# Performance work log

Measured on AMD Instinct MI355X. Metric: run time of the kernel, lower is better.

Reference implementation:

```python
import jax, jax.numpy as jnp
import numpy as np


def _lstm_layer(x, w_ih, w_hh, b, h0, c0):
    # x: [S, B, H]; w_ih, w_hh: [4H, H]; b: [4H] (b_ih + b_hh combined)
    H = h0.shape[-1]

    def step(carry, xt):
        h, c = carry
        gates = xt @ w_ih.T + h @ w_hh.T + b  # [B, 4H]
        i = jax.nn.sigmoid(gates[:, 0 * H:1 * H])
        f = jax.nn.sigmoid(gates[:, 1 * H:2 * H])
        g = jnp.tanh(gates[:, 2 * H:3 * H])
        o = jax.nn.sigmoid(gates[:, 3 * H:4 * H])
        c = f * c + i * g
        h = o * jnp.tanh(c)
        return (h, c), h

    (_, _), hs = jax.lax.scan(step, (h0, c0), x)
    return hs  # [S, B, H]


def setup_inputs() -> dict:
    key = jax.random.key(0)
    ks = jax.random.split(key, 5)
    S, B, H, L, C = 256, 64, 1024, 2, 10
    return {
        "x_data": jax.random.normal(ks[0], (S, B, H), dtype=jnp.float32),
        "weight": jax.random.normal(ks[1], (L, 2, 4 * H, H), dtype=jnp.float32) * 0.05,
        "bias": jax.random.normal(ks[2], (L, 2, 4 * H), dtype=jnp.float32) * 0.05,
        "fc_w": jax.random.normal(ks[3], (C, H), dtype=jnp.float32) * 0.05,
        "fc_b": jax.random.normal(ks[4], (C,), dtype=jnp.float32) * 0.05,
        "hiddenSize": H,
        "miniBatch": B,
        "seqLength": S,
        "numLayers": L,
    }


def reference(x_data, weight, bias, fc_w, fc_b, hiddenSize, miniBatch, seqLength, numLayers):
    B, H = miniBatch, hiddenSize
    h0 = jnp.zeros((B, H), dtype=x_data.dtype)
    c0 = jnp.zeros((B, H), dtype=x_data.dtype)
    x = x_data
    for layer in range(numLayers):
        w_ih = weight[layer, 0]  # [4H, H]
        w_hh = weight[layer, 1]  # [4H, H]
        b = bias[layer, 0] + bias[layer, 1]  # [4H]
        x = _lstm_layer(x, w_ih, w_hh, b, h0, c0)
    out = x[-1]  # last timestep of top layer: [B, H]
    return out @ fc_w.T + fc_b  # [B, num_classes]
```

## Files before the change

kernel.cpp:

```cpp
#include <hip/hip_runtime.h>
#include <cstdint>
#include <cstddef>

#define S_LEN 256
#define BATCH 64
#define HID   1024
#define GATES 4096
#define NBLK  256
#define RING_D 4

typedef _Float16 h16;
typedef _Float16 h16x8 __attribute__((ext_vector_type(8)));
typedef _Float16 h16x4 __attribute__((ext_vector_type(4)));
typedef float    f32x4 __attribute__((ext_vector_type(4)));

__global__ __launch_bounds__(256)
void xconv_kernel(const float* __restrict__ x, h16* __restrict__ x16)
{
  const int n4 = S_LEN * BATCH * HID / 4;
  const int stride = gridDim.x * 256;
  for (int i = blockIdx.x * 256 + threadIdx.x; i < n4; i += stride) {
    f32x4 v = ((const f32x4*)x)[i];
    h16x4 o;
    o[0] = (h16)v[0]; o[1] = (h16)v[1]; o[2] = (h16)v[2]; o[3] = (h16)v[3];
    ((h16x4*)x16)[i] = o;
  }
}

#define RLOAD(dst, ptr, OFFSTR)                                         \
  asm volatile("global_load_dwordx4 %0, %1, off offset:" OFFSTR " sc1"  \
               : "=&v"(dst) : "v"(ptr) : "memory")

__device__ __forceinline__ void wave_poll_c(const unsigned* grp, unsigned tgt)
{
  const unsigned* p = grp + (threadIdx.x & 63);
  while (true) {
    const unsigned u = __hip_atomic_load(p, __ATOMIC_RELAXED,
                                         __HIP_MEMORY_SCOPE_AGENT);
    if ((u & 0xffffu) >= tgt && (u >> 16) >= tgt) break;
    __builtin_amdgcn_s_sleep(1);
  }
}

__global__ __launch_bounds__(512, 1)
void lstm_persistent(const h16* __restrict__ x16,
                     const float* __restrict__ weight,
                     const float* __restrict__ bias,
                     h16* __restrict__ h0r,
                     h16* __restrict__ h1r,
                     unsigned* __restrict__ ep)
{
  __shared__ h16   wlds[65536];
  __shared__ float plds[2][8][16][32];

  const int wg    = blockIdx.x;
  const int layer = wg >> 7;
  const int j0    = (wg & 127) * 8;
  const int tid   = threadIdx.x;
  const int wave  = tid >> 6, lane = tid & 63;
  const int l15   = lane & 15, l16 = lane >> 4;
  const int BH    = BATCH * HID;

  {
    const float* wsrc = weight + (size_t)layer * 2 * GATES * HID;
    for (int c = tid; c < 8192; c += 512) {
      const int ln = c & 63, s = (c >> 6) & 3, n2 = (c >> 8) & 1,
                w = (c >> 9) & 7, part = c >> 12;
      const int lc  = n2 * 16 + (ln & 15);
      const int col = (lc >> 3) * HID + j0 + (lc & 7);
      const int k   = w * 128 + s * 32 + (ln >> 4) * 8;
      const float* p = wsrc + (part ? (size_t)GATES * HID : (size_t)0)
                            + (size_t)col * HID + k;
      h16x8 v;
#pragma unroll
      for (int e = 0; e < 8; ++e) v[e] = (h16)p[e];
      *(h16x8*)&wlds[(size_t)c * 8] = v;
    }
  }
  float bc[4];
  {
    const int j = tid & 7;
#pragma unroll
    for (int gg = 0; gg < 4; ++gg) {
      const int col = gg * HID + j0 + j;
      bc[gg] = bias[(size_t)layer * 2 * GATES + col] +
               bias[(size_t)layer * 2 * GATES + GATES + col];
    }
  }
  float creg2[2] = {0.f, 0.f};
  __syncthreads();

  const unsigned* ep_own = ep + layer * 64;
  const unsigned* ep_oth = ep + (1 - layer) * 64;
  unsigned short* my_ep  = (unsigned short*)ep + (size_t)layer * 128 + (wg & 127);
  const h16* bbI = wlds + (size_t)wave * 4096 + lane * 8;
  const h16* bbH = bbI + 32768;
  const int kw = wave * 128 + l16 * 8;

  for (int t = 0; t < S_LEN; ++t) {
    const h16* As;
    if (layer == 0) {
      As = x16 + (size_t)t * BH;
    } else {
      wave_poll_c(ep_oth, (unsigned)(t + 1));
      As = h0r + (size_t)(t % RING_D) * BH;
    }

    f32x4 accI[4][2];
#pragma unroll
    for (int i = 0; i < 4; ++i)
#pragma unroll
      for (int n2 = 0; n2 < 2; ++n2) accI[i][n2] = (f32x4)0.f;

#pragma unroll
    for (int sc = 0; sc < 2; ++sc) {
      h16x8 aS[2][4];
      if (layer == 0) {
#pragma unroll
        for (int ss = 0; ss < 2; ++ss)
#pragma unroll
          for (int i = 0; i < 4; ++i)
            aS[ss][i] = *(const h16x8*)(As + (size_t)(i * 16 + l15) * HID +
                                        kw + (sc * 2 + ss) * 32);
      } else {
#pragma unroll
        for (int i = 0; i < 4; ++i) {
          const h16* ap = As + (size_t)(i * 16 + l15) * HID + kw + sc * 64;
          RLOAD(aS[0][i], ap, "0");
          RLOAD(aS[1][i], ap, "64");
        }
        asm volatile("s_waitcnt vmcnt(0)" ::: "memory");
        __builtin_amdgcn_sched_barrier(0);
      }
#pragma unroll
      for (int ss = 0; ss < 2; ++ss) {
        const int s = sc * 2 + ss;
        const h16x8 b0 = *(const h16x8*)(bbI + s * 512);
        const h16x8 b1 = *(const h16x8*)(bbI + 2048 + s * 512);
#pragma unroll
        for (int i = 0; i < 4; ++i) {
          accI[i][0] = __builtin_amdgcn_mfma_f32_16x16x32_f16(aS[ss][i], b0, accI[i][0], 0, 0, 0);
          accI[i][1] = __builtin_amdgcn_mfma_f32_16x16x32_f16(aS[ss][i], b1, accI[i][1], 0, 0, 0);
        }
      }
    }

    if (t) wave_poll_c(ep_own, (unsigned)t);
    if (layer == 0) {
      const int ct = t + 1 - RING_D;
      if (ct > 0) wave_poll_c(ep_oth, (unsigned)ct);
    }

    const h16* Ah;
    h16* Hout;
    if (layer == 0) {
      Ah   = h0r + (size_t)((t + RING_D - 1) % RING_D) * BH;
      Hout = h0r + (size_t)(t % RING_D) * BH;
    } else {
      Ah   = h1r + (size_t)((t + 1) & 1) * BH;
      Hout = h1r + (size_t)(t & 1) * BH;
    }

    h16x8 aH[4][4];
#pragma unroll
    for (int i = 0; i < 4; ++i) {
      const h16* ap = Ah + (size_t)(i * 16 + l15) * HID + kw;
      RLOAD(aH[i][0], ap, "0");
      RLOAD(aH[i][1], ap, "64");
      RLOAD(aH[i][2], ap, "128");
      RLOAD(aH[i][3], ap, "192");
    }
    asm volatile("s_waitcnt vmcnt(0)" ::: "memory");
    __builtin_amdgcn_sched_barrier(0);

    f32x4 acc[4][2];
#pragma unroll
    for (int i = 0; i < 4; ++i)
#pragma unroll
      for (int n2 = 0; n2 < 2; ++n2) acc[i][n2] = accI[i][n2];

#pragma unroll
    for (int s = 0; s < 4; ++s) {
      const h16x8 b0 = *(const h16x8*)(bbH + s * 512);
      const h16x8 b1 = *(const h16x8*)(bbH + 2048 + s * 512);
#pragma unroll
      for (int i = 0; i < 4; ++i) {
        acc[i][0] = __builtin_amdgcn_mfma_f32_16x16x32_f16(aH[i][s], b0, acc[i][0], 0, 0, 0);
        acc[i][1] = __builtin_amdgcn_mfma_f32_16x16x32_f16(aH[i][s], b1, acc[i][1], 0, 0, 0);
      }
    }

#pragma unroll
    for (int p = 0; p < 2; ++p) {
#pragma unroll
      for (int ii = 0; ii < 2; ++ii) {
        const int i = p * 2 + ii;
#pragma unroll
        for (int n2 = 0; n2 < 2; ++n2)
#pragma unroll
          for (int q = 0; q < 4; ++q) {
            const int r = l16 * 4 + q;
            const int colS = (n2 * 16 + l15) ^ ((r & 7) << 2);
            plds[ii][wave][r][colS] = acc[i][n2][q];
          }
      }
      __syncthreads();
      if (tid < 256) {
        const int ii = tid >> 7, r = (tid >> 3) & 15, j = tid & 7;
        float gv[4];
#pragma unroll
        for (int gg = 0; gg < 4; ++gg) {
          const int colS = (gg * 8 + j) ^ ((r & 7) << 2);
          float s = bc[gg];
#pragma unroll
          for (int w = 0; w < 8; ++w) s += plds[ii][w][r][colS];
          gv[gg] = s;
        }
        const float ig = 1.f / (1.f + __expf(-gv[0]));
        const float fg = 1.f / (1.f + __expf(-gv[1]));
        const float gt = 1.f - 2.f / (__expf(2.f * gv[2]) + 1.f);
        const float og = 1.f / (1.f + __expf(-gv[3]));
        const float cn = fg * creg2[p] + ig * gt;
        creg2[p] = cn;
        const float th = 1.f - 2.f / (__expf(2.f * cn) + 1.f);
        union { h16 f; unsigned short u; } hb;
        hb.f = (h16)(og * th);
        const int row = (p * 2 + ii) * 16 + r;
        __hip_atomic_store(
            (unsigned short*)&Hout[(size_t)row * HID + j0 + j],
            hb.u, __ATOMIC_RELAXED, __HIP_MEMORY_SCOPE_AGENT);
      }
      __syncthreads();
    }

    if (tid == 0)
      asm volatile("global_store_short %0, %1, off sc1"
                   :: "v"(my_ep), "v"(t + 1) : "memory");
  }
}

__global__ __launch_bounds__(256)
void fc_kernel(const h16* __restrict__ h,
               const float* __restrict__ fw,
               const float* __restrict__ fb,
               float* __restrict__ out)
{
  const int gw = (blockIdx.x * blockDim.x + threadIdx.x) >> 6;
  const int lane = threadIdx.x & 63;
  if (gw >= BATCH * 10) return;
  const int m = gw / 10, cls = gw % 10;
  float s = 0.f;
  for (int k = lane; k < HID; k += 64)
    s += (float)h[(size_t)m * HID + k] * fw[(size_t)cls * HID + k];
#pragma unroll
  for (int off = 32; off; off >>= 1) s += __shfl_down(s, off);
  if (lane == 0) out[m * 10 + cls] = s + fb[cls];
}

extern "C" void kernel_launch(void* const* d_in, const int* in_sizes, int n_in,
                              void* d_out, int out_size, void* d_ws, size_t ws_size,
                              hipStream_t stream)
{
  const float* x      = (const float*)d_in[0];
  const float* weight = (const float*)d_in[1];
  const float* bias   = (const float*)d_in[2];
  const float* fc_w   = (const float*)d_in[3];
  const float* fc_b   = (const float*)d_in[4];
  float* out = (float*)d_out;

  auto align = [](size_t v) { return (v + 255) & ~(size_t)255; };
  const size_t ep_sz   = 512;
  const size_t x16_sz  = (size_t)S_LEN * BATCH * HID * sizeof(h16);
  const size_t h0r_sz  = (size_t)RING_D * BATCH * HID * sizeof(h16);
  const size_t h1r_sz  = (size_t)2 * BATCH * HID * sizeof(h16);

  char* p = (char*)d_ws;
  unsigned* ep = (unsigned*)p; p += align(ep_sz);
  h16* x16 = (h16*)p; p += align(x16_sz);
  h16* h0r = (h16*)p; p += align(h0r_sz);
  h16* h1r = (h16*)p; p += align(h1r_sz);

  hipMemsetAsync(ep, 0, ep_sz, stream);
  hipMemsetAsync(h0r, 0, h0r_sz, stream);
  hipMemsetAsync(h1r, 0, h1r_sz, stream);

  xconv_kernel<<<dim3(2048), 256, 0, stream>>>(x, x16);

  lstm_persistent<<<dim3(NBLK), dim3(512), 0, stream>>>(
      x16, weight, bias, h0r, h1r, ep);

  fc_kernel<<<dim3((BATCH * 10 * 64) / 256), 256, 0, stream>>>(
      h1r + (size_t)BATCH * HID, fc_w, fc_b, out);
}
```

Measured before the change: 2.410 ms.

## Halve persistent workgroups, keep only W_hh in LDS and stream fp16 W_ih

The persistent LSTM kernel now runs on 128 workgroups, each owning 16 hidden units instead of 8, so half as many blocks take part in each step's cross-block synchronisation. Only the recurrent weights fit in LDS at this width. The input-to-hidden weights are converted to fp16 once by a new kernel and read from global memory (L2) every timestep. This trades fewer synchronising participants and fewer epoch flags against per-step global weight traffic and using only half the CUs.

```diff
diff --git a/kernel.cpp b/kernel.cpp
--- a/kernel.cpp
+++ b/kernel.cpp
@@ -6,7 +6,7 @@
 #define BATCH 64
 #define HID   1024
 #define GATES 4096
-#define NBLK  256
+#define NBLK  128
 #define RING_D 4
 
 typedef _Float16 h16;
@@ -27,13 +27,29 @@
   }
 }
 
+__global__ __launch_bounds__(256)
+void wconv_kernel(const float* __restrict__ weight, h16* __restrict__ wih16)
+{
+  const int n4 = 2 * GATES * HID / 4;
+  const int stride = gridDim.x * 256;
+  for (int i = blockIdx.x * 256 + threadIdx.x; i < n4; i += stride) {
+    const int e = i * 4;
+    const int l = e >> 22;
+    const int r = e & ((GATES * HID) - 1);
+    f32x4 v = *(const f32x4*)(weight + (size_t)l * 2 * GATES * HID + r);
+    h16x4 o;
+    o[0] = (h16)v[0]; o[1] = (h16)v[1]; o[2] = (h16)v[2]; o[3] = (h16)v[3];
+    *(h16x4*)(wih16 + (size_t)l * GATES * HID + r) = o;
+  }
+}
+
 #define RLOAD(dst, ptr, OFFSTR)                                         \
   asm volatile("global_load_dwordx4 %0, %1, off offset:" OFFSTR " sc1"  \
                : "=&v"(dst) : "v"(ptr) : "memory")
 
 __device__ __forceinline__ void wave_poll_c(const unsigned* grp, unsigned tgt)
 {
-  const unsigned* p = grp + (threadIdx.x & 63);
+  const unsigned* p = grp + (threadIdx.x & 31);
   while (true) {
     const unsigned u = __hip_atomic_load(p, __ATOMIC_RELAXED,
                                          __HIP_MEMORY_SCOPE_AGENT);
@@ -44,6 +60,7 @@
 
 __global__ __launch_bounds__(512, 1)
 void lstm_persistent(const h16* __restrict__ x16,
+                     const h16* __restrict__ wih16,
                      const float* __restrict__ weight,
                      const float* __restrict__ bias,
                      h16* __restrict__ h0r,
@@ -51,26 +68,24 @@
                      unsigned* __restrict__ ep)
 {
   __shared__ h16   wlds[65536];
-  __shared__ float plds[2][8][16][32];
+  __shared__ float plds[8][16][64];
 
   const int wg    = blockIdx.x;
-  const int layer = wg >> 7;
-  const int j0    = (wg & 127) * 8;
+  const int layer = wg >> 6;
+  const int j0    = (wg & 63) * 16;
   const int tid   = threadIdx.x;
   const int wave  = tid >> 6, lane = tid & 63;
   const int l15   = lane & 15, l16 = lane >> 4;
   const int BH    = BATCH * HID;
 
   {
-    const float* wsrc = weight + (size_t)layer * 2 * GATES * HID;
+    const float* whh = weight + (size_t)layer * 2 * GATES * HID
+                              + (size_t)GATES * HID;
     for (int c = tid; c < 8192; c += 512) {
-      const int ln = c & 63, s = (c >> 6) & 3, n2 = (c >> 8) & 1,
-                w = (c >> 9) & 7, part = c >> 12;
-      const int lc  = n2 * 16 + (ln & 15);
-      const int col = (lc >> 3) * HID + j0 + (lc & 7);
+      const int ln = c & 63, s = (c >> 6) & 3, g = (c >> 8) & 3, w = c >> 10;
+      const int col = g * HID + j0 + (ln & 15);
       const int k   = w * 128 + s * 32 + (ln >> 4) * 8;
-      const float* p = wsrc + (part ? (size_t)GATES * HID : (size_t)0)
-                            + (size_t)col * HID + k;
+      const float* p = whh + (size_t)col * HID + k;
       h16x8 v;
 #pragma unroll
       for (int e = 0; e < 8; ++e) v[e] = (h16)p[e];
@@ -79,22 +94,22 @@
   }
   float bc[4];
   {
-    const int j = tid & 7;
+    const int jj = tid & 15;
 #pragma unroll
     for (int gg = 0; gg < 4; ++gg) {
-      const int col = gg * HID + j0 + j;
+      const int col = gg * HID + j0 + jj;
       bc[gg] = bias[(size_t)layer * 2 * GATES + col] +
                bias[(size_t)layer * 2 * GATES + GATES + col];
     }
   }
-  float creg2[2] = {0.f, 0.f};
+  float creg[4] = {0.f, 0.f, 0.f, 0.f};
   __syncthreads();
 
-  const unsigned* ep_own = ep + layer * 64;
-  const unsigned* ep_oth = ep + (1 - layer) * 64;
-  unsigned short* my_ep  = (unsigned short*)ep + (size_t)layer * 128 + (wg & 127);
-  const h16* bbI = wlds + (size_t)wave * 4096 + lane * 8;
-  const h16* bbH = bbI + 32768;
+  const unsigned* ep_own = ep + layer * 32;
+  const unsigned* ep_oth = ep + (1 - layer) * 32;
+  unsigned short* my_ep  = (unsigned short*)ep + (size_t)layer * 64 + (wg & 63);
+  const h16* wih = wih16 + (size_t)layer * GATES * HID;
+  const h16* bbH = wlds + (size_t)wave * 8192 + lane * 8;
   const int kw = wave * 128 + l16 * 8;
 
   for (int t = 0; t < S_LEN; ++t) {
@@ -106,50 +121,50 @@
       As = h0r + (size_t)(t % RING_D) * BH;
     }
 
-    f32x4 accI[4][2];
+    h16x8 aS[4][4], bS[4][4];
+#pragma unroll
+    for (int g = 0; g < 4; ++g) {
+      const h16* bp = wih + (size_t)(g * HID + j0 + l15) * HID + kw;
+#pragma unroll
+      for (int s = 0; s < 4; ++s) bS[g][s] = *(const h16x8*)(bp + s * 32);
+    }
+    if (layer == 0) {
+#pragma unroll
+      for (int i = 0; i < 4; ++i) {
+        const h16* ap = As + (size_t)(i * 16 + l15) * HID + kw;
+#pragma unroll
+        for (int s = 0; s < 4; ++s) aS[i][s] = *(const h16x8*)(ap + s * 32);
+      }
+    } else {
+#pragma unroll
+      for (int i = 0; i < 4; ++i) {
+        const h16* ap = As + (size_t)(i * 16 + l15) * HID + kw;
+        RLOAD(aS[i][0], ap, "0");
+        RLOAD(aS[i][1], ap, "64");
+        RLOAD(aS[i][2], ap, "128");
+        RLOAD(aS[i][3], ap, "192");
+      }
+      asm volatile("s_waitcnt vmcnt(0)" ::: "memory");
+      __builtin_amdgcn_sched_barrier(0);
+    }
+
+    f32x4 acc[4][4];
 #pragma unroll
     for (int i = 0; i < 4; ++i)
 #pragma unroll
-      for (int n2 = 0; n2 < 2; ++n2) accI[i][n2] = (f32x4)0.f;
-
-#pragma unroll
-    for (int sc = 0; sc < 2; ++sc) {
-      h16x8 aS[2][4];
-      if (layer == 0) {
-#pragma unroll
-        for (int ss = 0; ss < 2; ++ss)
-#pragma unroll
-          for (int i = 0; i < 4; ++i)
-            aS[ss][i] = *(const h16x8*)(As + (size_t)(i * 16 + l15) * HID +
-                                        kw + (sc * 2 + ss) * 32);
-      } else {
-#pragma unroll
-        for (int i = 0; i < 4; ++i) {
-          const h16* ap = As + (size_t)(i * 16 + l15) * HID + kw + sc * 64;
-          RLOAD(aS[0][i], ap, "0");
-          RLOAD(aS[1][i], ap, "64");
-        }
-        asm volatile("s_waitcnt vmcnt(0)" ::: "memory");
-        __builtin_amdgcn_sched_barrier(0);
-      }
-#pragma unroll
-      for (int ss = 0; ss < 2; ++ss) {
-        const int s = sc * 2 + ss;
-        const h16x8 b0 = *(const h16x8*)(bbI + s * 512);
-        const h16x8 b1 = *(const h16x8*)(bbI + 2048 + s * 512);
-#pragma unroll
-        for (int i = 0; i < 4; ++i) {
-          accI[i][0] = __builtin_amdgcn_mfma_f32_16x16x32_f16(aS[ss][i], b0, accI[i][0], 0, 0, 0);
-          accI[i][1] = __builtin_amdgcn_mfma_f32_16x16x32_f16(aS[ss][i], b1, accI[i][1], 0, 0, 0);
-        }
-      }
-    }
+      for (int g = 0; g < 4; ++g) acc[i][g] = (f32x4)0.f;
+
+#pragma unroll
+    for (int s = 0; s < 4; ++s)
+#pragma unroll
+      for (int i = 0; i < 4; ++i)
+#pragma unroll
+        for (int g = 0; g < 4; ++g)
+          acc[i][g] = __builtin_amdgcn_mfma_f32_16x16x32_f16(aS[i][s], bS[g][s],
+                                                             acc[i][g], 0, 0, 0);
 
     if (t) wave_poll_c(ep_own, (unsigned)t);
-    if (layer == 0) {
-      const int ct = t + 1 - RING_D;
-      if (ct > 0) wave_poll_c(ep_oth, (unsigned)ct);
-    }
+    if (layer == 0 && t >= RING_D) wave_poll_c(ep_oth, (unsigned)(t + 1 - RING_D));
 
     const h16* Ah;
     h16* Hout;
@@ -173,61 +188,51 @@
     asm volatile("s_waitcnt vmcnt(0)" ::: "memory");
     __builtin_amdgcn_sched_barrier(0);
 
-    f32x4 acc[4][2];
-#pragma unroll
-    for (int i = 0; i < 4; ++i)
-#pragma unroll
-      for (int n2 = 0; n2 < 2; ++n2) acc[i][n2] = accI[i][n2];
-
-#pragma unroll
-    for (int s = 0; s < 4; ++s) {
-      const h16x8 b0 = *(const h16x8*)(bbH + s * 512);
-      const h16x8 b1 = *(const h16x8*)(bbH + 2048 + s * 512);
-#pragma unroll
-      for (int i = 0; i < 4; ++i) {
-        acc[i][0] = __builtin_amdgcn_mfma_f32_16x16x32_f16(aH[i][s], b0, acc[i][0], 0, 0, 0);
-        acc[i][1] = __builtin_amdgcn_mfma_f32_16x16x32_f16(aH[i][s], b1, acc[i][1], 0, 0, 0);
+#pragma unroll
+    for (int s = 0; s < 4; ++s)
+#pragma unroll
+      for (int g = 0; g < 4; ++g) {
+        const h16x8 b = *(const h16x8*)(bbH + (g * 4 + s) * 512);
+#pragma unroll
+        for (int i = 0; i < 4; ++i)
+          acc[i][g] = __builtin_amdgcn_mfma_f32_16x16x32_f16(aH[i][s], b,
+                                                             acc[i][g], 0, 0, 0);
       }
-    }
-
-#pragma unroll
-    for (int p = 0; p < 2; ++p) {
-#pragma unroll
-      for (int ii = 0; ii < 2; ++ii) {
-        const int i = p * 2 + ii;
-#pragma unroll
-        for (int n2 = 0; n2 < 2; ++n2)
-#pragma unroll
-          for (int q = 0; q < 4; ++q) {
-            const int r = l16 * 4 + q;
-            const int colS = (n2 * 16 + l15) ^ ((r & 7) << 2);
-            plds[ii][wave][r][colS] = acc[i][n2][q];
-          }
-      }
+
+#pragma unroll
+    for (int p = 0; p < 4; ++p) {
+#pragma unroll
+      for (int g = 0; g < 4; ++g)
+#pragma unroll
+        for (int q = 0; q < 4; ++q) {
+          const int r = l16 * 4 + q;
+          const int colS = (g * 16 + l15) ^ ((r & 7) << 2);
+          plds[wave][r][colS] = acc[p][g][q];
+        }
       __syncthreads();
       if (tid < 256) {
-        const int ii = tid >> 7, r = (tid >> 3) & 15, j = tid & 7;
+        const int r = tid >> 4, jj = tid & 15;
         float gv[4];
 #pragma unroll
         for (int gg = 0; gg < 4; ++gg) {
-          const int colS = (gg * 8 + j) ^ ((r & 7) << 2);
+          const int colS = (gg * 16 + jj) ^ ((r & 7) << 2);
           float s = bc[gg];
 #pragma unroll
-          for (int w = 0; w < 8; ++w) s += plds[ii][w][r][colS];
+          for (int w = 0; w < 8; ++w) s += plds[w][r][colS];
           gv[gg] = s;
         }
         const float ig = 1.f / (1.f + __expf(-gv[0]));
         const float fg = 1.f / (1.f + __expf(-gv[1]));
         const float gt = 1.f - 2.f / (__expf(2.f * gv[2]) + 1.f);
         const float og = 1.f / (1.f + __expf(-gv[3]));
-        const float cn = fg * creg2[p] + ig * gt;
-        creg2[p] = cn;
+        const float cn = fg * creg[p] + ig * gt;
+        creg[p] = cn;
         const float th = 1.f - 2.f / (__expf(2.f * cn) + 1.f);
         union { h16 f; unsigned short u; } hb;
         hb.f = (h16)(og * th);
-        const int row = (p * 2 + ii) * 16 + r;
+        const int row = p * 16 + r;
         __hip_atomic_store(
-            (unsigned short*)&Hout[(size_t)row * HID + j0 + j],
+            (unsigned short*)&Hout[(size_t)row * HID + j0 + jj],
             hb.u, __ATOMIC_RELAXED, __HIP_MEMORY_SCOPE_AGENT);
       }
       __syncthreads();
@@ -269,25 +274,28 @@
   float* out = (float*)d_out;
 
   auto align = [](size_t v) { return (v + 255) & ~(size_t)255; };
-  const size_t ep_sz   = 512;
-  const size_t x16_sz  = (size_t)S_LEN * BATCH * HID * sizeof(h16);
-  const size_t h0r_sz  = (size_t)RING_D * BATCH * HID * sizeof(h16);
-  const size_t h1r_sz  = (size_t)2 * BATCH * HID * sizeof(h16);
+  const size_t ep_sz    = 512;
+  const size_t x16_sz   = (size_t)S_LEN * BATCH * HID * sizeof(h16);
+  const size_t wih_sz   = (size_t)2 * GATES * HID * sizeof(h16);
+  const size_t h0r_sz   = (size_t)RING_D * BATCH * HID * sizeof(h16);
+  const size_t h1r_sz   = (size_t)2 * BATCH * HID * sizeof(h16);
 
   char* p = (char*)d_ws;
   unsigned* ep = (unsigned*)p; p += align(ep_sz);
-  h16* x16 = (h16*)p; p += align(x16_sz);
-  h16* h0r = (h16*)p; p += align(h0r_sz);
-  h16* h1r = (h16*)p; p += align(h1r_sz);
+  h16* x16   = (h16*)p; p += align(x16_sz);
+  h16* wih16 = (h16*)p; p += align(wih_sz);
+  h16* h0r   = (h16*)p; p += align(h0r_sz);
+  h16* h1r   = (h16*)p; p += align(h1r_sz);
 
   hipMemsetAsync(ep, 0, ep_sz, stream);
   hipMemsetAsync(h0r, 0, h0r_sz, stream);
   hipMemsetAsync(h1r, 0, h1r_sz, stream);
 
   xconv_kernel<<<dim3(2048), 256, 0, stream>>>(x, x16);
+  wconv_kernel<<<dim3(2048), 256, 0, stream>>>(weight, wih16);
 
   lstm_persistent<<<dim3(NBLK), dim3(512), 0, stream>>>(
-      x16, weight, bias, h0r, h1r, ep);
+      x16, wih16, weight, bias, h0r, h1r, ep);
 
   fc_kernel<<<dim3((BATCH * 10 * 64) / 256), 256, 0, stream>>>(
       h1r + (size_t)BATCH * HID, fc_w, fc_b, out);
```

Result: slower. 3.001 ms (+24.5%).
